# Kernel tuning notes

Measured on AMD Instinct MI355X. Metric: run time of the kernel, lower is better.

The kernel has to match this reference:

```python
import jax, jax.numpy as jnp
import numpy as np

DIM_V = 512
H = 8
EPS = 1e-5

def _layernorm(x, g, b):
    mu = jnp.mean(x, axis=-1, keepdims=True)
    var = jnp.var(x, axis=-1, keepdims=True)
    return (x - mu) * jax.lax.rsqrt(var + EPS) * g + b

def setup_inputs() -> dict:
    key = jax.random.key(0)
    ks = jax.random.split(key, 10)
    B, Nq, Nk, dq, dk, dv = 8, 1024, 1024, 512, 512, DIM_V
    def lin(k, fan_in, shape):
        bound = 1.0 / np.sqrt(fan_in)
        return jax.random.uniform(k, shape, jnp.float32, -bound, bound)
    return {
        "Q": jax.random.normal(ks[0], (B, Nq, dq), jnp.float32),
        "K": jax.random.normal(ks[1], (B, Nk, dk), jnp.float32),
        "Wq": lin(ks[2], dq, (dv, dq)), "bq": lin(ks[3], dq, (dv,)),
        "Wk": lin(ks[4], dk, (dv, dk)), "bk": lin(ks[5], dk, (dv,)),
        "Wv": lin(ks[6], dk, (dv, dk)), "bv": lin(ks[7], dk, (dv,)),
        "Wo": lin(ks[8], dv, (dv, dv)), "bo": lin(ks[9], dv, (dv,)),
        "g0": jnp.ones((dv,), jnp.float32), "beta0": jnp.zeros((dv,), jnp.float32),
        "g1": jnp.ones((dv,), jnp.float32), "beta1": jnp.zeros((dv,), jnp.float32),
    }

def reference(Q, K, Wq, bq, Wk, bk, Wv, bv, Wo, bo, g0, beta0, g1, beta1):
    B, Nq, _ = Q.shape
    Nk = K.shape[1]
    d_h = DIM_V // H
    Qp = Q @ Wq.T + bq            # [B,Nq,dv]
    Kp = K @ Wk.T + bk            # [B,Nk,dv]
    Vp = K @ Wv.T + bv            # [B,Nk,dv]
    # split heads along feature dim (matches torch split(dim_split,2)+cat(0))
    Qh = Qp.reshape(B, Nq, H, d_h).transpose(0, 2, 1, 3)  # [B,H,Nq,dh]
    Kh = Kp.reshape(B, Nk, H, d_h).transpose(0, 2, 1, 3)
    Vh = Vp.reshape(B, Nk, H, d_h).transpose(0, 2, 1, 3)
    # NOTE: original scales by sqrt(dim_V), the FULL model dim
    scores = jnp.einsum('bhnd,bhmd->bhnm', Qh, Kh) / jnp.sqrt(jnp.float32(DIM_V))
    A = jax.nn.softmax(scores, axis=-1)                   # [B,H,Nq,Nk]
    Oh = Qh + jnp.einsum('bhnm,bhmd->bhnd', A, Vh)        # residual on projected Q
    O = Oh.transpose(0, 2, 1, 3).reshape(B, Nq, DIM_V)
    O = _layernorm(O, g0, beta0)
    O = O + jax.nn.relu(O @ Wo.T + bo)
    O = _layernorm(O, g1, beta1)
    return O
```

## Files before the change

kernel.cpp:

```cpp
#include <hip/hip_runtime.h>
#include <hip/hip_bf16.h>

typedef __hip_bfloat16 bf16;
typedef short bf16x8 __attribute__((ext_vector_type(8)));
typedef float f32x4 __attribute__((ext_vector_type(4)));
typedef unsigned int u32;

static __device__ __forceinline__ float bfu2f(unsigned short u) { return __uint_as_float((u32)u << 16); }
static __device__ __forceinline__ u32 pack2(float a, float b) {
    return (u32)__bfloat16_as_ushort(__float2bfloat16(a))
         | ((u32)__bfloat16_as_ushort(__float2bfloat16(b)) << 16);
}
static __device__ __forceinline__ float wave_sum(float v) {
    #pragma unroll
    for (int off = 32; off > 0; off >>= 1) v += __shfl_xor(v, off);
    return v;
}

#define LDSK 40

__global__ __launch_bounds__(256) void gemm_f32(const float* __restrict__ A,
                                                const float* __restrict__ W0, const float* __restrict__ W1,
                                                const float* __restrict__ b0, const float* __restrict__ b1,
                                                bf16* __restrict__ o0, bf16* __restrict__ o1,
                                                int m0, int m1)
{
    __shared__ bf16 As[64 * LDSK];
    __shared__ bf16 Bs[64 * LDSK];

    const int tid = threadIdx.x, lane = tid & 63, wave = tid >> 6;
    const int yy = blockIdx.y;
    const float* W    = yy < 8 ? W0 : W1;
    const float* bias = yy < 8 ? b0 : b1;
    bf16* out         = yy < 8 ? o0 : o1;
    const int mode    = yy < 8 ? m0 : m1;
    const int bm = blockIdx.x * 64;
    const int bn = (yy < 8 ? yy : yy - 8) * 64;

    const int lrow = tid >> 2, lcol = (tid & 3) * 8;
    const int wm = (wave >> 1) * 32, wn = (wave & 1) * 32;
    const int fr = lane & 15, kq = (lane >> 4) * 8;

    f32x4 acc[2][2] = {};
    const float* Ap = A + (size_t)(bm + lrow) * 512 + lcol;
    const float* Wp = W + (size_t)(bn + lrow) * 512 + lcol;

    for (int k0 = 0; k0 < 512; k0 += 32) {
        const float4 a0 = *(const float4*)(Ap + k0), a1 = *(const float4*)(Ap + k0 + 4);
        const float4 w0 = *(const float4*)(Wp + k0), w1 = *(const float4*)(Wp + k0 + 4);
        uint4 ap, wp;
        ap.x = pack2(a0.x, a0.y); ap.y = pack2(a0.z, a0.w);
        ap.z = pack2(a1.x, a1.y); ap.w = pack2(a1.z, a1.w);
        wp.x = pack2(w0.x, w0.y); wp.y = pack2(w0.z, w0.w);
        wp.z = pack2(w1.x, w1.y); wp.w = pack2(w1.z, w1.w);
        __syncthreads();
        *(uint4*)(&As[lrow * LDSK + lcol]) = ap;
        *(uint4*)(&Bs[lrow * LDSK + lcol]) = wp;
        __syncthreads();

        bf16x8 fa0 = *(const bf16x8*)(&As[(wm      + fr) * LDSK + kq]);
        bf16x8 fa1 = *(const bf16x8*)(&As[(wm + 16 + fr) * LDSK + kq]);
        bf16x8 fb0 = *(const bf16x8*)(&Bs[(wn      + fr) * LDSK + kq]);
        bf16x8 fb1 = *(const bf16x8*)(&Bs[(wn + 16 + fr) * LDSK + kq]);

        acc[0][0] = __builtin_amdgcn_mfma_f32_16x16x32_bf16(fa0, fb0, acc[0][0], 0, 0, 0);
        acc[0][1] = __builtin_amdgcn_mfma_f32_16x16x32_bf16(fa0, fb1, acc[0][1], 0, 0, 0);
        acc[1][0] = __builtin_amdgcn_mfma_f32_16x16x32_bf16(fa1, fb0, acc[1][0], 0, 0, 0);
        acc[1][1] = __builtin_amdgcn_mfma_f32_16x16x32_bf16(fa1, fb1, acc[1][1], 0, 0, 0);
    }

    const int r0 = (lane >> 4) * 4;
    #pragma unroll
    for (int i = 0; i < 2; i++) {
        #pragma unroll
        for (int j = 0; j < 2; j++) {
            const int col = bn + wn + j * 16 + fr;
            const float bv = bias[col];
            #pragma unroll
            for (int r = 0; r < 4; r++) {
                const int row = bm + wm + i * 16 + r0 + r;
                const float v = acc[i][j][r] + bv;
                const int b = row >> 10, n = row & 1023;
                const int h = col >> 6,  d = col & 63;
                size_t idx;
                if (mode == 1) idx = ((size_t)(b * 8 + h) * 1024 + n) * 64 + d;
                else           idx = ((size_t)(b * 8 + h) * 64 + d) * 1024 + n;
                out[idx] = __float2bfloat16(v);
            }
        }
    }
}

__global__ __launch_bounds__(256) void gemm_of(const bf16* __restrict__ A,
                                               const float* __restrict__ W,
                                               const float* __restrict__ bias,
                                               bf16* __restrict__ out)
{
    __shared__ bf16 As[64 * LDSK];
    __shared__ bf16 Bs[64 * LDSK];

    const int tid = threadIdx.x, lane = tid & 63, wave = tid >> 6;
    const int bm = blockIdx.x * 64;
    const int bn = blockIdx.y * 64;

    const int lrow = tid >> 2, lcol = (tid & 3) * 8;
    const int wm = (wave >> 1) * 32, wn = (wave & 1) * 32;
    const int fr = lane & 15, kq = (lane >> 4) * 8;

    f32x4 acc[2][2] = {};
    const bf16* Ap = A + (size_t)(bm + lrow) * 512 + lcol;
    const float* Wp = W + (size_t)(bn + lrow) * 512 + lcol;

    for (int k0 = 0; k0 < 512; k0 += 32) {
        const int4 av = *(const int4*)(Ap + k0);
        const float4 w0 = *(const float4*)(Wp + k0), w1 = *(const float4*)(Wp + k0 + 4);
        uint4 wp;
        wp.x = pack2(w0.x, w0.y); wp.y = pack2(w0.z, w0.w);
        wp.z = pack2(w1.x, w1.y); wp.w = pack2(w1.z, w1.w);
        __syncthreads();
        *(int4*)(&As[lrow * LDSK + lcol]) = av;
        *(uint4*)(&Bs[lrow * LDSK + lcol]) = wp;
        __syncthreads();

        bf16x8 fa0 = *(const bf16x8*)(&As[(wm      + fr) * LDSK + kq]);
        bf16x8 fa1 = *(const bf16x8*)(&As[(wm + 16 + fr) * LDSK + kq]);
        bf16x8 fb0 = *(const bf16x8*)(&Bs[(wn      + fr) * LDSK + kq]);
        bf16x8 fb1 = *(const bf16x8*)(&Bs[(wn + 16 + fr) * LDSK + kq]);

        acc[0][0] = __builtin_amdgcn_mfma_f32_16x16x32_bf16(fa0, fb0, acc[0][0], 0, 0, 0);
        acc[0][1] = __builtin_amdgcn_mfma_f32_16x16x32_bf16(fa0, fb1, acc[0][1], 0, 0, 0);
        acc[1][0] = __builtin_amdgcn_mfma_f32_16x16x32_bf16(fa1, fb0, acc[1][0], 0, 0, 0);
        acc[1][1] = __builtin_amdgcn_mfma_f32_16x16x32_bf16(fa1, fb1, acc[1][1], 0, 0, 0);
    }

    const int r0 = (lane >> 4) * 4;
    #pragma unroll
    for (int i = 0; i < 2; i++) {
        #pragma unroll
        for (int j = 0; j < 2; j++) {
            const int col = bn + wn + j * 16 + fr;
            const float bv = bias[col];
            #pragma unroll
            for (int r = 0; r < 4; r++) {
                const int row = bm + wm + i * 16 + r0 + r;
                out[(size_t)row * 512 + col] = __float2bfloat16(acc[i][j][r] + bv);
            }
        }
    }
}

__global__ __launch_bounds__(256) void attn_mfma(const bf16* __restrict__ Qh,
                                                 const bf16* __restrict__ Kh,
                                                 const bf16* __restrict__ VhT,
                                                 bf16* __restrict__ Oc)
{
    __shared__ bf16 Ks[2 * 64 * 32];
    __shared__ bf16 Vs[2 * 64 * 32];
    __shared__ bf16 Ps[4][16 * 72];

    const int tid = threadIdx.x, lane = tid & 63, w = tid >> 6;
    const int bh = blockIdx.y;
    const int wq = blockIdx.x * 64 + w * 16;

    const bf16* Qb = Qh  + ((size_t)bh * 1024 + wq) * 64;
    const bf16* Kb = Kh  + (size_t)bh * 1024 * 64;
    const bf16* Vb = VhT + (size_t)bh * 64 * 1024;

    const int fl = lane & 15, fq = lane >> 4;

    bf16x8 qf0 = *(const bf16x8*)(Qb + fl * 64 + fq * 8);
    bf16x8 qf1 = *(const bf16x8*)(Qb + fl * 64 + 32 + fq * 8);

    f32x4 o[4] = {};
    float mr2 = -1e30f, lr = 0.f;
    const float sc2 = 0.04419417382415922f * 1.4426950408889634f;

    const int srow = tid >> 3;
    const int seq  = tid & 7;
    const int scc = seq >> 2, sq8 = (seq & 3) * 8;

    for (int kt = 0; kt < 16; kt++) {
        const int m0 = kt * 64;
        const int4 kv0 = *(const int4*)(Kb + (size_t)(m0 + srow) * 64 + seq * 8);
        const int4 kv1 = *(const int4*)(Kb + (size_t)(m0 + srow + 32) * 64 + seq * 8);
        const int4 vv0 = *(const int4*)(Vb + (size_t)srow * 1024 + m0 + seq * 8);
        const int4 vv1 = *(const int4*)(Vb + (size_t)(srow + 32) * 1024 + m0 + seq * 8);
        __syncthreads();
        *(int4*)(&Ks[(scc * 64 + srow) * 32 + sq8])      = kv0;
        *(int4*)(&Ks[(scc * 64 + srow + 32) * 32 + sq8]) = kv1;
        *(int4*)(&Vs[(scc * 64 + srow) * 32 + sq8])      = vv0;
        *(int4*)(&Vs[(scc * 64 + srow + 32) * 32 + sq8]) = vv1;
        __syncthreads();

        f32x4 st[4] = {};
        #pragma unroll
        for (int tm = 0; tm < 4; tm++) {
            bf16x8 kf0 = *(const bf16x8*)(&Ks[(     16 * tm + fl) * 32 + fq * 8]);
            bf16x8 kf1 = *(const bf16x8*)(&Ks[(64 + 16 * tm + fl) * 32 + fq * 8]);
            st[tm] = __builtin_amdgcn_mfma_f32_16x16x32_bf16(kf0, qf0, st[tm], 0, 0, 0);
            st[tm] = __builtin_amdgcn_mfma_f32_16x16x32_bf16(kf1, qf1, st[tm], 0, 0, 0);
        }

        float cm = st[0][0];
        #pragma unroll
        for (int tm = 0; tm < 4; tm++)
            #pragma unroll
            for (int r = 0; r < 4; r++) cm = fmaxf(cm, st[tm][r]);
        cm = fmaxf(cm, __shfl_xor(cm, 16));
        cm = fmaxf(cm, __shfl_xor(cm, 32));
        const float mnew2 = fmaxf(mr2, cm * sc2);
        const float alpha = __builtin_amdgcn_exp2f(mr2 - mnew2);
        mr2 = mnew2;

        float psum = 0.f;
        float p[4][4];
        #pragma unroll
        for (int tm = 0; tm < 4; tm++)
            #pragma unroll
            for (int r = 0; r < 4; r++) {
                p[tm][r] = __builtin_amdgcn_exp2f(fmaf(st[tm][r], sc2, -mnew2));
                psum += p[tm][r];
            }
        psum += __shfl_xor(psum, 16);
        psum += __shfl_xor(psum, 32);
        lr = lr * alpha + psum;

        #pragma unroll
        for (int jd = 0; jd < 4; jd++)
            #pragma unroll
            for (int r = 0; r < 4; r++) o[jd][r] *= alpha;

        #pragma unroll
        for (int tm = 0; tm < 4; tm++) {
            uint2 pk;
            pk.x = pack2(p[tm][0], p[tm][1]);
            pk.y = pack2(p[tm][2], p[tm][3]);
            *(uint2*)(&Ps[w][fl * 72 + 16 * tm + fq * 4]) = pk;
        }

        bf16x8 pf0 = *(const bf16x8*)(&Ps[w][fl * 72 +      fq * 8]);
        bf16x8 pf1 = *(const bf16x8*)(&Ps[w][fl * 72 + 32 + fq * 8]);
        #pragma unroll
        for (int jd = 0; jd < 4; jd++) {
            bf16x8 vf0 = *(const bf16x8*)(&Vs[(     16 * jd + fl) * 32 + fq * 8]);
            bf16x8 vf1 = *(const bf16x8*)(&Vs[(64 + 16 * jd + fl) * 32 + fq * 8]);
            o[jd] = __builtin_amdgcn_mfma_f32_16x16x32_bf16(vf0, pf0, o[jd], 0, 0, 0);
            o[jd] = __builtin_amdgcn_mfma_f32_16x16x32_bf16(vf1, pf1, o[jd], 0, 0, 0);
        }
    }

    const float linv = 1.f / lr;
    const int b = bh >> 3, h = bh & 7;
    const size_t obase = ((size_t)(b * 1024 + wq + fl)) * 512 + h * 64;
    #pragma unroll
    for (int jd = 0; jd < 4; jd++) {
        const ushort4 qr = *(const ushort4*)(Qb + fl * 64 + 16 * jd + fq * 4);
        const float v0 = o[jd][0] * linv + bfu2f(qr.x);
        const float v1 = o[jd][1] * linv + bfu2f(qr.y);
        const float v2 = o[jd][2] * linv + bfu2f(qr.z);
        const float v3 = o[jd][3] * linv + bfu2f(qr.w);
        uint2 w2;
        w2.x = pack2(v0, v1);
        w2.y = pack2(v2, v3);
        *(uint2*)(&Oc[obase + 16 * jd + fq * 4]) = w2;
    }
}

__global__ __launch_bounds__(256) void ln0(const bf16* __restrict__ X,
                                           const float* __restrict__ g,
                                           const float* __restrict__ be,
                                           bf16* __restrict__ Y)
{
    const int lane = threadIdx.x & 63;
    const int row = blockIdx.x * 4 + (threadIdx.x >> 6);
    const size_t base = (size_t)row * 512 + lane * 8;
    const bf16x8 xv = *(const bf16x8*)(X + base);
    float x[8];
    #pragma unroll
    for (int j = 0; j < 8; j++) x[j] = bfu2f((unsigned short)xv[j]);
    float s = 0.f, s2 = 0.f;
    #pragma unroll
    for (int j = 0; j < 8; j++) { s += x[j]; s2 += x[j] * x[j]; }
    s = wave_sum(s); s2 = wave_sum(s2);
    const float mean = s * (1.f / 512.f);
    const float var = s2 * (1.f / 512.f) - mean * mean;
    const float rs = rsqrtf(fmaxf(var, 0.f) + 1e-5f);
    const float4 gv0 = *(const float4*)(g + lane * 8);
    const float4 gv1 = *(const float4*)(g + lane * 8 + 4);
    const float4 bv0 = *(const float4*)(be + lane * 8);
    const float4 bv1 = *(const float4*)(be + lane * 8 + 4);
    uint4 ov;
    ov.x = pack2((x[0]-mean)*rs*gv0.x + bv0.x, (x[1]-mean)*rs*gv0.y + bv0.y);
    ov.y = pack2((x[2]-mean)*rs*gv0.z + bv0.z, (x[3]-mean)*rs*gv0.w + bv0.w);
    ov.z = pack2((x[4]-mean)*rs*gv1.x + bv1.x, (x[5]-mean)*rs*gv1.y + bv1.y);
    ov.w = pack2((x[6]-mean)*rs*gv1.z + bv1.z, (x[7]-mean)*rs*gv1.w + bv1.w);
    *(uint4*)(Y + base) = ov;
}

__global__ __launch_bounds__(256) void ln1(const bf16* __restrict__ X,
                                           const bf16* __restrict__ R,
                                           const float* __restrict__ g,
                                           const float* __restrict__ be,
                                           float* __restrict__ Y)
{
    const int lane = threadIdx.x & 63;
    const int row = blockIdx.x * 4 + (threadIdx.x >> 6);
    const size_t base = (size_t)row * 512 + lane * 8;
    const bf16x8 xv = *(const bf16x8*)(X + base);
    const bf16x8 rv = *(const bf16x8*)(R + base);
    float x[8];
    #pragma unroll
    for (int j = 0; j < 8; j++)
        x[j] = bfu2f((unsigned short)rv[j]) + fmaxf(bfu2f((unsigned short)xv[j]), 0.f);
    float s = 0.f, s2 = 0.f;
    #pragma unroll
    for (int j = 0; j < 8; j++) { s += x[j]; s2 += x[j] * x[j]; }
    s = wave_sum(s); s2 = wave_sum(s2);
    const float mean = s * (1.f / 512.f);
    const float var = s2 * (1.f / 512.f) - mean * mean;
    const float rs = rsqrtf(fmaxf(var, 0.f) + 1e-5f);
    const float4 gv0 = *(const float4*)(g + lane * 8);
    const float4 gv1 = *(const float4*)(g + lane * 8 + 4);
    const float4 bv0 = *(const float4*)(be + lane * 8);
    const float4 bv1 = *(const float4*)(be + lane * 8 + 4);
    float4 y0, y1;
    y0.x = (x[0]-mean)*rs*gv0.x + bv0.x; y0.y = (x[1]-mean)*rs*gv0.y + bv0.y;
    y0.z = (x[2]-mean)*rs*gv0.z + bv0.z; y0.w = (x[3]-mean)*rs*gv0.w + bv0.w;
    y1.x = (x[4]-mean)*rs*gv1.x + bv1.x; y1.y = (x[5]-mean)*rs*gv1.y + bv1.y;
    y1.z = (x[6]-mean)*rs*gv1.z + bv1.z; y1.w = (x[7]-mean)*rs*gv1.w + bv1.w;
    *(float4*)(Y + base)     = y0;
    *(float4*)(Y + base + 4) = y1;
}

extern "C" void kernel_launch(void* const* d_in, const int* in_sizes, int n_in,
                              void* d_out, int out_size, void* d_ws, size_t ws_size,
                              hipStream_t stream)
{
    const float* Q   = (const float*)d_in[0];
    const float* K   = (const float*)d_in[1];
    const float* Wq  = (const float*)d_in[2];
    const float* bq  = (const float*)d_in[3];
    const float* Wk  = (const float*)d_in[4];
    const float* bk  = (const float*)d_in[5];
    const float* Wv  = (const float*)d_in[6];
    const float* bv  = (const float*)d_in[7];
    const float* Wo  = (const float*)d_in[8];
    const float* bo  = (const float*)d_in[9];
    const float* g0  = (const float*)d_in[10];
    const float* be0 = (const float*)d_in[11];
    const float* g1  = (const float*)d_in[12];
    const float* be1 = (const float*)d_in[13];
    float* out = (float*)d_out;

    const size_t NQK = (size_t)8 * 1024 * 512;
    bf16* ws   = (bf16*)d_ws;
    bf16* pQh  = ws;
    bf16* pKh  = ws + NQK;
    bf16* pVhT = ws + 2 * NQK;
    bf16* pOc  = (bf16*)d_out;
    bf16* pO1  = pKh;
    bf16* pTmp = pQh;

    gemm_f32<<<dim3(128, 8),  256, 0, stream>>>(Q, Wq, Wq, bq, bq, pQh, pQh, 1, 1);
    gemm_f32<<<dim3(128, 16), 256, 0, stream>>>(K, Wk, Wv, bk, bv, pKh, pVhT, 1, 2);
    attn_mfma<<<dim3(16, 64), 256, 0, stream>>>(pQh, pKh, pVhT, pOc);
    ln0<<<2048, 256, 0, stream>>>(pOc, g0, be0, pO1);
    gemm_of<<<dim3(128, 8), 256, 0, stream>>>(pO1, Wo, bo, pTmp);
    ln1<<<2048, 256, 0, stream>>>(pTmp, pO1, g1, be1, out);
}
```

Measured before the change: 214.2 us.

## Pre-cast inputs and weights to bf16, use 128x128 GEMM tiles, repad attention LDS

Adds a single cast kernel that converts Q, K and all four weight matrices to bf16 up front. The projection and output GEMMs are replaced by one 128x128-tile kernel where each wave computes a 64x64 block with 16 MFMAs per k-step, raising operand reuse and halving global reads of fp32 data. The attention K/V shared-memory layout changes to padded rows of stride 72. The trade-offs are an extra launch and extra round-trip traffic for the casts, more accumulator registers, and fewer blocks (256 or 512) on a large GPU, which may leave compute units idle.

```diff
diff --git a/kernel.cpp b/kernel.cpp
--- a/kernel.cpp
+++ b/kernel.cpp
@@ -17,133 +17,111 @@
     return v;
 }
 
+__global__ __launch_bounds__(256) void castall(const float* __restrict__ Q,  const float* __restrict__ K,
+                                               const float* __restrict__ Wq, const float* __restrict__ Wk,
+                                               const float* __restrict__ Wv, const float* __restrict__ Wo,
+                                               bf16* __restrict__ dQ,  bf16* __restrict__ dK,
+                                               bf16* __restrict__ dWq, bf16* __restrict__ dWk,
+                                               bf16* __restrict__ dWv, bf16* __restrict__ dWo)
+{
+    const int b = blockIdx.x;
+    const float* src; bf16* dst; size_t off;
+    if (b < 1024)      { src = Q;  dst = dQ;  off = (size_t)b * 4096; }
+    else if (b < 2048) { src = K;  dst = dK;  off = (size_t)(b - 1024) * 4096; }
+    else {
+        const int wb = b - 2048, wi = wb >> 6;
+        off = (size_t)(wb & 63) * 4096;
+        src = wi == 0 ? Wq : wi == 1 ? Wk : wi == 2 ? Wv : Wo;
+        dst = wi == 0 ? dWq : wi == 1 ? dWk : wi == 2 ? dWv : dWo;
+    }
+    const size_t p = off + threadIdx.x * 16;
+    const float4 v0 = *(const float4*)(src + p);
+    const float4 v1 = *(const float4*)(src + p + 4);
+    const float4 v2 = *(const float4*)(src + p + 8);
+    const float4 v3 = *(const float4*)(src + p + 12);
+    uint4 o0, o1;
+    o0.x = pack2(v0.x, v0.y); o0.y = pack2(v0.z, v0.w);
+    o0.z = pack2(v1.x, v1.y); o0.w = pack2(v1.z, v1.w);
+    o1.x = pack2(v2.x, v2.y); o1.y = pack2(v2.z, v2.w);
+    o1.z = pack2(v3.x, v3.y); o1.w = pack2(v3.z, v3.w);
+    *(uint4*)(dst + p)     = o0;
+    *(uint4*)(dst + p + 8) = o1;
+}
+
 #define LDSK 40
 
-__global__ __launch_bounds__(256) void gemm_f32(const float* __restrict__ A,
-                                                const float* __restrict__ W0, const float* __restrict__ W1,
-                                                const float* __restrict__ b0, const float* __restrict__ b1,
-                                                bf16* __restrict__ o0, bf16* __restrict__ o1,
-                                                int m0, int m1)
-{
-    __shared__ bf16 As[64 * LDSK];
-    __shared__ bf16 Bs[64 * LDSK];
+__global__ __launch_bounds__(256) void gemm128(const bf16* __restrict__ A,
+                                               const bf16* __restrict__ W0, const bf16* __restrict__ W1,
+                                               const float* __restrict__ b0, const float* __restrict__ b1,
+                                               bf16* __restrict__ o0, bf16* __restrict__ o1,
+                                               int m0, int m1, int ny)
+{
+    __shared__ bf16 As[128 * LDSK];
+    __shared__ bf16 Bs[128 * LDSK];
 
     const int tid = threadIdx.x, lane = tid & 63, wave = tid >> 6;
     const int yy = blockIdx.y;
-    const float* W    = yy < 8 ? W0 : W1;
-    const float* bias = yy < 8 ? b0 : b1;
-    bf16* out         = yy < 8 ? o0 : o1;
-    const int mode    = yy < 8 ? m0 : m1;
-    const int bm = blockIdx.x * 64;
-    const int bn = (yy < 8 ? yy : yy - 8) * 64;
+    const bf16* W     = yy < ny ? W0 : W1;
+    const float* bias = yy < ny ? b0 : b1;
+    bf16* out         = yy < ny ? o0 : o1;
+    const int mode    = yy < ny ? m0 : m1;
+    const int bm = blockIdx.x * 128;
+    const int bn = (yy < ny ? yy : yy - ny) * 128;
 
     const int lrow = tid >> 2, lcol = (tid & 3) * 8;
-    const int wm = (wave >> 1) * 32, wn = (wave & 1) * 32;
+    const int wm = (wave >> 1) * 64, wn = (wave & 1) * 64;
     const int fr = lane & 15, kq = (lane >> 4) * 8;
 
-    f32x4 acc[2][2] = {};
-    const float* Ap = A + (size_t)(bm + lrow) * 512 + lcol;
-    const float* Wp = W + (size_t)(bn + lrow) * 512 + lcol;
+    f32x4 acc[4][4] = {};
+    const bf16* Ap = A + (size_t)(bm + lrow) * 512 + lcol;
+    const bf16* Wp = W + (size_t)(bn + lrow) * 512 + lcol;
 
     for (int k0 = 0; k0 < 512; k0 += 32) {
-        const float4 a0 = *(const float4*)(Ap + k0), a1 = *(const float4*)(Ap + k0 + 4);
-        const float4 w0 = *(const float4*)(Wp + k0), w1 = *(const float4*)(Wp + k0 + 4);
-        uint4 ap, wp;
-        ap.x = pack2(a0.x, a0.y); ap.y = pack2(a0.z, a0.w);
-        ap.z = pack2(a1.x, a1.y); ap.w = pack2(a1.z, a1.w);
-        wp.x = pack2(w0.x, w0.y); wp.y = pack2(w0.z, w0.w);
-        wp.z = pack2(w1.x, w1.y); wp.w = pack2(w1.z, w1.w);
+        const int4 av0 = *(const int4*)(Ap + k0);
+        const int4 av1 = *(const int4*)(Ap + k0 + (size_t)64 * 512);
+        const int4 wv0 = *(const int4*)(Wp + k0);
+        const int4 wv1 = *(const int4*)(Wp + k0 + (size_t)64 * 512);
         __syncthreads();
-        *(uint4*)(&As[lrow * LDSK + lcol]) = ap;
-        *(uint4*)(&Bs[lrow * LDSK + lcol]) = wp;
+        *(int4*)(&As[lrow * LDSK + lcol])        = av0;
+        *(int4*)(&As[(lrow + 64) * LDSK + lcol]) = av1;
+        *(int4*)(&Bs[lrow * LDSK + lcol])        = wv0;
+        *(int4*)(&Bs[(lrow + 64) * LDSK + lcol]) = wv1;
         __syncthreads();
 
-        bf16x8 fa0 = *(const bf16x8*)(&As[(wm      + fr) * LDSK + kq]);
-        bf16x8 fa1 = *(const bf16x8*)(&As[(wm + 16 + fr) * LDSK + kq]);
-        bf16x8 fb0 = *(const bf16x8*)(&Bs[(wn      + fr) * LDSK + kq]);
-        bf16x8 fb1 = *(const bf16x8*)(&Bs[(wn + 16 + fr) * LDSK + kq]);
-
-        acc[0][0] = __builtin_amdgcn_mfma_f32_16x16x32_bf16(fa0, fb0, acc[0][0], 0, 0, 0);
-        acc[0][1] = __builtin_amdgcn_mfma_f32_16x16x32_bf16(fa0, fb1, acc[0][1], 0, 0, 0);
-        acc[1][0] = __builtin_amdgcn_mfma_f32_16x16x32_bf16(fa1, fb0, acc[1][0], 0, 0, 0);
-        acc[1][1] = __builtin_amdgcn_mfma_f32_16x16x32_bf16(fa1, fb1, acc[1][1], 0, 0, 0);
+        bf16x8 fa[4], fb[4];
+        #pragma unroll
+        for (int i = 0; i < 4; i++) {
+            fa[i] = *(const bf16x8*)(&As[(wm + 16 * i + fr) * LDSK + kq]);
+            fb[i] = *(const bf16x8*)(&Bs[(wn + 16 * i + fr) * LDSK + kq]);
+        }
+        #pragma unroll
+        for (int i = 0; i < 4; i++)
+            #pragma unroll
+            for (int j = 0; j < 4; j++)
+                acc[i][j] = __builtin_amdgcn_mfma_f32_16x16x32_bf16(fa[i], fb[j], acc[i][j], 0, 0, 0);
     }
 
     const int r0 = (lane >> 4) * 4;
     #pragma unroll
-    for (int i = 0; i < 2; i++) {
-        #pragma unroll
-        for (int j = 0; j < 2; j++) {
-            const int col = bn + wn + j * 16 + fr;
+    for (int i = 0; i < 4; i++) {
+        #pragma unroll
+        for (int j = 0; j < 4; j++) {
+            const int col = bn + wn + 16 * j + fr;
             const float bv = bias[col];
             #pragma unroll
             for (int r = 0; r < 4; r++) {
-                const int row = bm + wm + i * 16 + r0 + r;
+                const int row = bm + wm + 16 * i + r0 + r;
                 const float v = acc[i][j][r] + bv;
-                const int b = row >> 10, n = row & 1023;
-                const int h = col >> 6,  d = col & 63;
                 size_t idx;
-                if (mode == 1) idx = ((size_t)(b * 8 + h) * 1024 + n) * 64 + d;
-                else           idx = ((size_t)(b * 8 + h) * 64 + d) * 1024 + n;
+                if (mode == 0) {
+                    idx = (size_t)row * 512 + col;
+                } else {
+                    const int b = row >> 10, n = row & 1023;
+                    const int h = col >> 6,  d = col & 63;
+                    if (mode == 1) idx = ((size_t)(b * 8 + h) * 1024 + n) * 64 + d;
+                    else           idx = ((size_t)(b * 8 + h) * 64 + d) * 1024 + n;
+                }
                 out[idx] = __float2bfloat16(v);
-            }
-        }
-    }
-}
-
-__global__ __launch_bounds__(256) void gemm_of(const bf16* __restrict__ A,
-                                               const float* __restrict__ W,
-                                               const float* __restrict__ bias,
-                                               bf16* __restrict__ out)
-{
-    __shared__ bf16 As[64 * LDSK];
-    __shared__ bf16 Bs[64 * LDSK];
-
-    const int tid = threadIdx.x, lane = tid & 63, wave = tid >> 6;
-    const int bm = blockIdx.x * 64;
-    const int bn = blockIdx.y * 64;
-
-    const int lrow = tid >> 2, lcol = (tid & 3) * 8;
-    const int wm = (wave >> 1) * 32, wn = (wave & 1) * 32;
-    const int fr = lane & 15, kq = (lane >> 4) * 8;
-
-    f32x4 acc[2][2] = {};
-    const bf16* Ap = A + (size_t)(bm + lrow) * 512 + lcol;
-    const float* Wp = W + (size_t)(bn + lrow) * 512 + lcol;
-
-    for (int k0 = 0; k0 < 512; k0 += 32) {
-        const int4 av = *(const int4*)(Ap + k0);
-        const float4 w0 = *(const float4*)(Wp + k0), w1 = *(const float4*)(Wp + k0 + 4);
-        uint4 wp;
-        wp.x = pack2(w0.x, w0.y); wp.y = pack2(w0.z, w0.w);
-        wp.z = pack2(w1.x, w1.y); wp.w = pack2(w1.z, w1.w);
-        __syncthreads();
-        *(int4*)(&As[lrow * LDSK + lcol]) = av;
-        *(uint4*)(&Bs[lrow * LDSK + lcol]) = wp;
-        __syncthreads();
-
-        bf16x8 fa0 = *(const bf16x8*)(&As[(wm      + fr) * LDSK + kq]);
-        bf16x8 fa1 = *(const bf16x8*)(&As[(wm + 16 + fr) * LDSK + kq]);
-        bf16x8 fb0 = *(const bf16x8*)(&Bs[(wn      + fr) * LDSK + kq]);
-        bf16x8 fb1 = *(const bf16x8*)(&Bs[(wn + 16 + fr) * LDSK + kq]);
-
-        acc[0][0] = __builtin_amdgcn_mfma_f32_16x16x32_bf16(fa0, fb0, acc[0][0], 0, 0, 0);
-        acc[0][1] = __builtin_amdgcn_mfma_f32_16x16x32_bf16(fa0, fb1, acc[0][1], 0, 0, 0);
-        acc[1][0] = __builtin_amdgcn_mfma_f32_16x16x32_bf16(fa1, fb0, acc[1][0], 0, 0, 0);
-        acc[1][1] = __builtin_amdgcn_mfma_f32_16x16x32_bf16(fa1, fb1, acc[1][1], 0, 0, 0);
-    }
-
-    const int r0 = (lane >> 4) * 4;
-    #pragma unroll
-    for (int i = 0; i < 2; i++) {
-        #pragma unroll
-        for (int j = 0; j < 2; j++) {
-            const int col = bn + wn + j * 16 + fr;
-            const float bv = bias[col];
-            #pragma unroll
-            for (int r = 0; r < 4; r++) {
-                const int row = bm + wm + i * 16 + r0 + r;
-                out[(size_t)row * 512 + col] = __float2bfloat16(acc[i][j][r] + bv);
             }
         }
     }
@@ -154,8 +132,8 @@
                                                  const bf16* __restrict__ VhT,
                                                  bf16* __restrict__ Oc)
 {
-    __shared__ bf16 Ks[2 * 64 * 32];
-    __shared__ bf16 Vs[2 * 64 * 32];
+    __shared__ bf16 Ks[64 * 72];
+    __shared__ bf16 Vs[64 * 72];
     __shared__ bf16 Ps[4][16 * 72];
 
     const int tid = threadIdx.x, lane = tid & 63, w = tid >> 6;
@@ -175,9 +153,8 @@
     float mr2 = -1e30f, lr = 0.f;
     const float sc2 = 0.04419417382415922f * 1.4426950408889634f;
 
-    const int srow = tid >> 3;
+    const int srow = (tid >> 3) & 31;
     const int seq  = tid & 7;
-    const int scc = seq >> 2, sq8 = (seq & 3) * 8;
 
     for (int kt = 0; kt < 16; kt++) {
         const int m0 = kt * 64;
@@ -186,17 +163,17 @@
         const int4 vv0 = *(const int4*)(Vb + (size_t)srow * 1024 + m0 + seq * 8);
         const int4 vv1 = *(const int4*)(Vb + (size_t)(srow + 32) * 1024 + m0 + seq * 8);
         __syncthreads();
-        *(int4*)(&Ks[(scc * 64 + srow) * 32 + sq8])      = kv0;
-        *(int4*)(&Ks[(scc * 64 + srow + 32) * 32 + sq8]) = kv1;
-        *(int4*)(&Vs[(scc * 64 + srow) * 32 + sq8])      = vv0;
-        *(int4*)(&Vs[(scc * 64 + srow + 32) * 32 + sq8]) = vv1;
+        *(int4*)(&Ks[srow * 72 + seq * 8])        = kv0;
+        *(int4*)(&Ks[(srow + 32) * 72 + seq * 8]) = kv1;
+        *(int4*)(&Vs[srow * 72 + seq * 8])        = vv0;
+        *(int4*)(&Vs[(srow + 32) * 72 + seq * 8]) = vv1;
         __syncthreads();
 
         f32x4 st[4] = {};
         #pragma unroll
         for (int tm = 0; tm < 4; tm++) {
-            bf16x8 kf0 = *(const bf16x8*)(&Ks[(     16 * tm + fl) * 32 + fq * 8]);
-            bf16x8 kf1 = *(const bf16x8*)(&Ks[(64 + 16 * tm + fl) * 32 + fq * 8]);
+            bf16x8 kf0 = *(const bf16x8*)(&Ks[(16 * tm + fl) * 72 + fq * 8]);
+            bf16x8 kf1 = *(const bf16x8*)(&Ks[(16 * tm + fl) * 72 + 32 + fq * 8]);
             st[tm] = __builtin_amdgcn_mfma_f32_16x16x32_bf16(kf0, qf0, st[tm], 0, 0, 0);
             st[tm] = __builtin_amdgcn_mfma_f32_16x16x32_bf16(kf1, qf1, st[tm], 0, 0, 0);
         }
@@ -238,12 +215,12 @@
             *(uint2*)(&Ps[w][fl * 72 + 16 * tm + fq * 4]) = pk;
         }
 
-        bf16x8 pf0 = *(const bf16x8*)(&Ps[w][fl * 72 +      fq * 8]);
+        bf16x8 pf0 = *(const bf16x8*)(&Ps[w][fl * 72 + fq * 8]);
         bf16x8 pf1 = *(const bf16x8*)(&Ps[w][fl * 72 + 32 + fq * 8]);
         #pragma unroll
         for (int jd = 0; jd < 4; jd++) {
-            bf16x8 vf0 = *(const bf16x8*)(&Vs[(     16 * jd + fl) * 32 + fq * 8]);
-            bf16x8 vf1 = *(const bf16x8*)(&Vs[(64 + 16 * jd + fl) * 32 + fq * 8]);
+            bf16x8 vf0 = *(const bf16x8*)(&Vs[(16 * jd + fl) * 72 + fq * 8]);
+            bf16x8 vf1 = *(const bf16x8*)(&Vs[(16 * jd + fl) * 72 + 32 + fq * 8]);
             o[jd] = __builtin_amdgcn_mfma_f32_16x16x32_bf16(vf0, pf0, o[jd], 0, 0, 0);
             o[jd] = __builtin_amdgcn_mfma_f32_16x16x32_bf16(vf1, pf1, o[jd], 0, 0, 0);
         }
@@ -353,18 +330,26 @@
     float* out = (float*)d_out;
 
     const size_t NQK = (size_t)8 * 1024 * 512;
+    const size_t NW  = (size_t)512 * 512;
     bf16* ws   = (bf16*)d_ws;
-    bf16* pQh  = ws;
-    bf16* pKh  = ws + NQK;
-    bf16* pVhT = ws + 2 * NQK;
+    bf16* cQ   = ws;
+    bf16* cK   = cQ + NQK;
+    bf16* cWq  = cK + NQK;
+    bf16* cWk  = cWq + NW;
+    bf16* cWv  = cWk + NW;
+    bf16* cWo  = cWv + NW;
+    bf16* pQh  = cWo + NW;
+    bf16* pKh  = pQh + NQK;
+    bf16* pVhT = pKh + NQK;
     bf16* pOc  = (bf16*)d_out;
     bf16* pO1  = pKh;
     bf16* pTmp = pQh;
 
-    gemm_f32<<<dim3(128, 8),  256, 0, stream>>>(Q, Wq, Wq, bq, bq, pQh, pQh, 1, 1);
-    gemm_f32<<<dim3(128, 16), 256, 0, stream>>>(K, Wk, Wv, bk, bv, pKh, pVhT, 1, 2);
+    castall<<<2304, 256, 0, stream>>>(Q, K, Wq, Wk, Wv, Wo, cQ, cK, cWq, cWk, cWv, cWo);
+    gemm128<<<dim3(64, 4), 256, 0, stream>>>(cQ, cWq, cWq, bq, bq, pQh, pQh, 1, 1, 4);
+    gemm128<<<dim3(64, 8), 256, 0, stream>>>(cK, cWk, cWv, bk, bv, pKh, pVhT, 1, 2, 4);
     attn_mfma<<<dim3(16, 64), 256, 0, stream>>>(pQh, pKh, pVhT, pOc);
     ln0<<<2048, 256, 0, stream>>>(pOc, g0, be0, pO1);
-    gemm_of<<<dim3(128, 8), 256, 0, stream>>>(pO1, Wo, bo, pTmp);
+    gemm128<<<dim3(64, 4), 256, 0, stream>>>(pO1, cWo, cWo, bo, bo, pTmp, pTmp, 0, 0, 4);
     ln1<<<2048, 256, 0, stream>>>(pTmp, pO1, g1, be1, out);
 }
```

After: 212.6 us. Within noise of the previous version (-0.7%).
